# Optimization experiments

Measured on AMD Instinct MI355X. Metric: run time of the kernel, lower is better.

Reference implementation:

```python
import jax, jax.numpy as jnp
import numpy as np

N, E, F, H, O = 50000, 800000, 64, 128, 64
GRID_SIZE, SPLINE_ORDER = 3, 2


def make_grid(in_features, grid_size=GRID_SIZE, spline_order=SPLINE_ORDER, grid_range=(-1.0, 1.0)):
    h = (grid_range[1] - grid_range[0]) / grid_size
    pts = jnp.arange(-spline_order, grid_size + spline_order + 1, dtype=jnp.float32) * h + grid_range[0]
    return jnp.tile(pts[None, :], (in_features, 1))  # [in, grid_size + 2*order + 1]


def b_splines(x, grid, spline_order=SPLINE_ORDER):
    # x: [B, in], grid: [in, G+2k+1] -> bases [B, in, G+k]
    xe = x[..., None]
    bases = ((xe >= grid[:, :-1]) & (xe < grid[:, 1:])).astype(x.dtype)
    for k in range(1, spline_order + 1):
        bases = ((xe - grid[:, : -(k + 1)]) / (grid[:, k:-1] - grid[:, : -(k + 1)]) * bases[..., :-1]
                 + (grid[:, k + 1:] - xe) / (grid[:, k + 1:] - grid[:, 1:-k]) * bases[..., 1:])
    return bases


def setup_inputs() -> dict:
    key = jax.random.key(0)
    ks = jax.random.split(key, 12)
    x = jax.random.normal(ks[0], (N, F), dtype=jnp.float32)
    contexts = jax.random.normal(ks[1], (E, F), dtype=jnp.float32)
    attn = jax.random.uniform(ks[2], (E,), dtype=jnp.float32)
    seg_ids = jnp.sort(jax.random.randint(ks[3], (E,), 0, N, dtype=jnp.int32))
    s = 0.05
    Wn = jax.random.normal(ks[4], (H, F), dtype=jnp.float32) * s
    bn = jnp.zeros((H,), dtype=jnp.float32)
    Wc = jax.random.normal(ks[5], (H, F), dtype=jnp.float32) * s
    bc = jnp.zeros((H,), dtype=jnp.float32)
    Wu = jax.random.normal(ks[6], (O, H), dtype=jnp.float32) * s
    bu = jnp.zeros((O,), dtype=jnp.float32)
    n_coef = GRID_SIZE + SPLINE_ORDER
    base_w = jax.random.normal(ks[7], (O, O), dtype=jnp.float32) * s
    spline_w = jax.random.normal(ks[8], (O, O, n_coef), dtype=jnp.float32) * s
    spline_scaler = jnp.ones((O, O), dtype=jnp.float32)
    grid = make_grid(O)
    return dict(x=x, contexts=contexts, attn=attn, seg_ids=seg_ids, Wn=Wn, bn=bn,
                Wc=Wc, bc=bc, Wu=Wu, bu=bu, base_w=base_w, spline_w=spline_w,
                spline_scaler=spline_scaler, grid=grid)


def reference(x, contexts, attn, seg_ids, Wn, bn, Wc, bc, Wu, bu, base_w, spline_w, spline_scaler, grid):
    n = x.shape[0]
    # per-edge context transform, attention weighting
    ctx_t = contexts @ Wc.T + bc                      # [E, H]
    weighted = ctx_t * attn[:, None]                  # [E, H]
    seg_sum = jax.ops.segment_sum(weighted, seg_ids, num_segments=n)        # [N, H]
    deg = jax.ops.segment_sum(jnp.ones_like(attn), seg_ids, num_segments=n)  # [N]
    ctx_agg = seg_sum / jnp.maximum(deg, 1.0)[:, None]  # mean over edges per node
    x_t = x @ Wn.T + bn                               # [N, H]
    upd = (x_t + ctx_agg) @ Wu.T + bu                 # [N, O]
    # KANLinear (efficient-kan): silu base path + b-spline path
    base_out = jax.nn.silu(upd) @ base_w.T            # [N, O]
    bases = b_splines(upd, grid)                      # [N, O, G+k]
    scaled_sw = spline_w * spline_scaler[..., None]   # [O, O, G+k]
    spline_out = jnp.einsum('bik,oik->bo', bases, scaled_sw)
    kan_out = base_out + spline_out
    # nodes with no contexts keep their raw features (num_features == output_dim)
    return jnp.where(deg[:, None] > 0, kan_out, x)
```

## Files before the change

kernel.cpp:

```cpp
#include <hip/hip_runtime.h>
#include <hip/hip_bf16.h>

#define NN 50000
#define NE 800000

typedef short short8 __attribute__((ext_vector_type(8)));
typedef float f32x4 __attribute__((ext_vector_type(4)));
typedef unsigned short ushort_t;

static __device__ __forceinline__ unsigned bits(float f) { return __float_as_uint(f); }
static __device__ __forceinline__ float hi_f(float v) {
  return __uint_as_float(bits(v) & 0xFFFF0000u);
}
static __device__ __forceinline__ ushort_t hi_u(float v) { return (ushort_t)(bits(v) >> 16); }
static __device__ __forceinline__ unsigned pack_hi(float v0, float v1) {
  return (bits(v0) >> 16) | (bits(v1) & 0xFFFF0000u);
}
static __device__ __forceinline__ unsigned pack_lo(float v0, float v1) {
  float l0 = v0 - hi_f(v0), l1 = v1 - hi_f(v1);
  return (bits(l0) >> 16) | (bits(l1) & 0xFFFF0000u);
}

#define MFMA(a, b, c) __builtin_amdgcn_mfma_f32_16x16x32_bf16(a, b, c, 0, 0, 0)

__global__ __launch_bounds__(256) void kA_pack_off(
    const float* __restrict__ Wn, const float* __restrict__ Wc,
    const float* __restrict__ Wu, const float* __restrict__ base_w,
    const float* __restrict__ spline_w, const float* __restrict__ scaler,
    const int* __restrict__ seg,
    ushort_t* __restrict__ p1h, ushort_t* __restrict__ p2h,
    ushort_t* __restrict__ p3h, int* __restrict__ off) {
  int t = blockIdx.x * 256 + threadIdx.x;
  if (t < 4096) {
    int l = t & 63, lm = l & 15, lk = l >> 4;
    if (t < 2048) {
      int nt = t >> 8, ks = (t >> 6) & 3;
      int h = nt * 16 + lm;
#pragma unroll
      for (int j = 0; j < 8; ++j) {
        int f = ks * 32 + lk * 8 + j;
        float v = (f < 64) ? Wn[h * 64 + f] : Wc[h * 64 + (f - 64)];
        p1h[t * 8 + j] = hi_u(v);
      }
    }
    if (t < 1024) {
      int nt = t >> 8, ks = (t >> 6) & 3;
      int o = nt * 16 + lm;
#pragma unroll
      for (int j = 0; j < 8; ++j) {
        int hh = ks * 32 + lk * 8 + j;
        p2h[t * 8 + j] = hi_u(Wu[o * 128 + hh]);
      }
    }
    if (t < 3072) {
      int nt = t / 768, ks = (t >> 6) % 12;
      int o = nt * 16 + lm;
#pragma unroll
      for (int j = 0; j < 8; ++j) {
        int k = ks * 32 + lk * 8 + j;
        int i = k / 6, c = k % 6;
        float v = (c == 0) ? base_w[o * 64 + i]
                           : spline_w[(o * 64 + i) * 5 + (c - 1)] * scaler[o * 64 + i];
        p3h[t * 8 + j] = hi_u(v);
      }
    }
  }
  int e = t;
  if (e < NE) {
    int s1 = seg[e];
    if (e == 0) {
      for (int n = 0; n <= s1; ++n) off[n] = 0;
    } else {
      int s0 = seg[e - 1];
      for (int n = s0 + 1; n <= s1; ++n) off[n] = e;
    }
    if (e == NE - 1) {
      for (int n = s1 + 1; n <= NN; ++n) off[n] = NE;
    }
  }
}

__global__ __launch_bounds__(512, 4) void k1234(
    const float* __restrict__ x,
    const float* __restrict__ contexts, const float* __restrict__ attn,
    const int* __restrict__ off,
    const float* __restrict__ bn, const float* __restrict__ bc,
    const float* __restrict__ bu,
    const ushort_t* __restrict__ p1h, const ushort_t* __restrict__ p2h,
    const ushort_t* __restrict__ p3h,
    const float* __restrict__ gridp, float* __restrict__ out) {
  __shared__ __align__(16) unsigned char arena[49152];
  __shared__ float ap[64], degl[64];
  ushort_t* Uh = (ushort_t*)arena;
  ushort_t* Ul = (ushort_t*)(arena + 16384);
  ushort_t* Th = (ushort_t*)(arena + 32768);
  ushort_t* Vh = (ushort_t*)arena;

  int tid = threadIdx.x;
  int n0 = blockIdx.x * 64;
  int w = tid >> 6, l = tid & 63;
  int wm = w >> 2, wn = w & 3;
  int lm = l & 15, lk = l >> 4;
  const short8* P1h = (const short8*)p1h;
  const short8* P2h = (const short8*)p2h;
  const short8* P3h = (const short8*)p3h;

  {
    const float4* x4 = (const float4*)x;
    int row = tid >> 3, slot = tid & 7;
    int n = n0 + row;
    float4 a = make_float4(0.f, 0.f, 0.f, 0.f), b = a;
    if (n < NN) {
      a = x4[(size_t)n * 16 + slot * 2];
      b = x4[(size_t)n * 16 + slot * 2 + 1];
    }
    uint4 hp, lp;
    hp.x = pack_hi(a.x, a.y); hp.y = pack_hi(a.z, a.w);
    hp.z = pack_hi(b.x, b.y); hp.w = pack_hi(b.z, b.w);
    lp.x = pack_lo(a.x, a.y); lp.y = pack_lo(a.z, a.w);
    lp.z = pack_lo(b.x, b.y); lp.w = pack_lo(b.z, b.w);
    int idx = (row * 128 + slot * 8) ^ ((row & 7) << 3);
    *(uint4*)&Uh[idx] = hp;
    *(uint4*)&Ul[idx] = lp;
  }

  {
    int nb = n0 + w * 8;
    int offv = 0;
    if (l < 9) offv = off[min(nb + l, NN)];
    int sub = l >> 4, fq = l & 15;
    const float4* ctx4 = (const float4*)contexts;
#pragma unroll 1
    for (int i = 0; i < 8; ++i) {
      int s = __shfl(offv, i);
      int e_end = __shfl(offv, i + 1);
      int deg_i = e_end - s;
      float4 S = make_float4(0.f, 0.f, 0.f, 0.f);
      float A = 0.f;
      if (deg_i > 0) {
        int last = e_end - 1;
        for (int e0 = s; e0 < e_end; e0 += 16) {
          float a[4];
          float4 c[4];
#pragma unroll
          for (int u = 0; u < 4; ++u) {
            int eu = e0 + 4 * u + sub;
            a[u] = (eu < e_end) ? attn[eu] : 0.f;
            c[u] = ctx4[(size_t)min(eu, last) * 16 + fq];
          }
#pragma unroll
          for (int u = 0; u < 4; ++u) {
            S.x += a[u] * c[u].x;
            S.y += a[u] * c[u].y;
            S.z += a[u] * c[u].z;
            S.w += a[u] * c[u].w;
            A += a[u];
          }
        }
      }
#pragma unroll
      for (int m = 16; m <= 32; m <<= 1) {
        S.x += __shfl_xor(S.x, m);
        S.y += __shfl_xor(S.y, m);
        S.z += __shfl_xor(S.z, m);
        S.w += __shfl_xor(S.w, m);
        A += __shfl_xor(A, m);
      }
      float deg = (float)deg_i;
      float inv = 1.f / fmaxf(deg, 1.f);
      int row = w * 8 + i;
      if (l < 16) {
        float ox = S.x * inv, oy = S.y * inv, oz = S.z * inv, ow = S.w * inv;
        uint2 hp, lp;
        hp.x = pack_hi(ox, oy);
        hp.y = pack_hi(oz, ow);
        lp.x = pack_lo(ox, oy);
        lp.y = pack_lo(oz, ow);
        int idx = (row * 128 + 64 + l * 4) ^ ((row & 7) << 3);
        *(uint2*)&Uh[idx] = hp;
        *(uint2*)&Ul[idx] = lp;
      }
      if (l == 0) { ap[row] = A * inv; degl[row] = deg; }
    }
  }

  short8 B1[2][4], B2[4];
#pragma unroll
  for (int q = 0; q < 2; ++q)
#pragma unroll
    for (int ks = 0; ks < 4; ++ks) B1[q][ks] = P1h[((2 * wn + q) * 4 + ks) * 64 + l];
#pragma unroll
  for (int ks = 0; ks < 4; ++ks) B2[ks] = P2h[(wn * 4 + ks) * 64 + l];

  __syncthreads();

  int swzA = (lm & 7) << 3;

  f32x4 acc1[2][2];
#pragma unroll
  for (int q = 0; q < 2; ++q)
#pragma unroll
    for (int ms = 0; ms < 2; ++ms) acc1[q][ms] = (f32x4){0.f, 0.f, 0.f, 0.f};
#pragma unroll
  for (int ks = 0; ks < 4; ++ks) {
    short8 ah[2], al[2];
#pragma unroll
    for (int ms = 0; ms < 2; ++ms) {
      int ai = (((2 * wm + ms) * 16 + lm) * 128 + ks * 32 + lk * 8) ^ swzA;
      ah[ms] = *(const short8*)&Uh[ai];
      al[ms] = *(const short8*)&Ul[ai];
    }
#pragma unroll
    for (int q = 0; q < 2; ++q)
#pragma unroll
      for (int ms = 0; ms < 2; ++ms) {
        acc1[q][ms] = MFMA(ah[ms], B1[q][ks], acc1[q][ms]);
        acc1[q][ms] = MFMA(al[ms], B1[q][ks], acc1[q][ms]);
      }
  }
#pragma unroll
  for (int q = 0; q < 2; ++q) {
    int h = (2 * wn + q) * 16 + lm;
    float bnv = bn[h], bcv = bc[h];
#pragma unroll
    for (int ms = 0; ms < 2; ++ms) {
#pragma unroll
      for (int r = 0; r < 4; ++r) {
        int node = (2 * wm + ms) * 16 + lk * 4 + r;
        float t = acc1[q][ms][r] + bnv + ap[node] * bcv;
        Th[(node * 128 + h) ^ ((node & 7) << 3)] = hi_u(t);
      }
    }
  }
  __syncthreads();

  short8 B3[12];
#pragma unroll
  for (int ks = 0; ks < 12; ++ks) B3[ks] = P3h[(wn * 12 + ks) * 64 + l];
  float g[8];
#pragma unroll
  for (int j = 0; j < 8; ++j) g[j] = gridp[j];
  float r1[7], r2[6];
#pragma unroll
  for (int j = 0; j < 7; ++j) r1[j] = 1.f / (g[j + 1] - g[j]);
#pragma unroll
  for (int j = 0; j < 6; ++j) r2[j] = 1.f / (g[j + 2] - g[j]);
  float buv = bu[wn * 16 + lm];

  f32x4 acc2[2];
  acc2[0] = (f32x4){0.f, 0.f, 0.f, 0.f};
  acc2[1] = (f32x4){0.f, 0.f, 0.f, 0.f};
#pragma unroll
  for (int ks = 0; ks < 4; ++ks) {
#pragma unroll
    for (int ms = 0; ms < 2; ++ms) {
      int ai = (((2 * wm + ms) * 16 + lm) * 128 + ks * 32 + lk * 8) ^ swzA;
      short8 ah = *(const short8*)&Th[ai];
      acc2[ms] = MFMA(ah, B2[ks], acc2[ms]);
    }
  }

#pragma unroll
  for (int half = 0; half < 2; ++half) {
    if (wm == half) {
#pragma unroll
      for (int ms = 0; ms < 2; ++ms) {
#pragma unroll
        for (int r = 0; r < 4; ++r) {
          float xv = acc2[ms][r] + buv;
          float sil = xv / (1.f + __expf(-xv));
          float b0[7], b1[6], b2[5];
#pragma unroll
          for (int q = 0; q < 7; ++q) b0[q] = (xv >= g[q] && xv < g[q + 1]) ? 1.f : 0.f;
#pragma unroll
          for (int q = 0; q < 6; ++q)
            b1[q] = (xv - g[q]) * r1[q] * b0[q] + (g[q + 2] - xv) * r1[q + 1] * b0[q + 1];
#pragma unroll
          for (int q = 0; q < 5; ++q)
            b2[q] = (xv - g[q]) * r2[q] * b1[q] + (g[q + 3] - xv) * r2[q + 1] * b1[q + 1];
          int ln = ms * 16 + lk * 4 + r;
          int base = ln * 392 + (wn * 16 + lm) * 6;
          *(unsigned*)&Vh[base + 0] = pack_hi(sil, b2[0]);
          *(unsigned*)&Vh[base + 2] = pack_hi(b2[1], b2[2]);
          *(unsigned*)&Vh[base + 4] = pack_hi(b2[3], b2[4]);
        }
      }
    }
    __syncthreads();

    f32x4 accK = (f32x4){0.f, 0.f, 0.f, 0.f};
#pragma unroll
    for (int ks = 0; ks < 12; ++ks) {
      short8 ah = *(const short8*)&Vh[(wm * 16 + lm) * 392 + ks * 32 + lk * 8];
      accK = MFMA(ah, B3[ks], accK);
    }
    if (half == 0) __syncthreads();

    int o = wn * 16 + lm;
#pragma unroll
    for (int r = 0; r < 4; ++r) {
      int node = half * 32 + wm * 16 + lk * 4 + r;
      int n = n0 + node;
      if (n < NN) {
        float val = accK[r];
        if (degl[node] <= 0.f) val = x[(size_t)n * 64 + o];
        out[(size_t)n * 64 + o] = val;
      }
    }
  }
}

extern "C" void kernel_launch(void* const* d_in, const int* in_sizes, int n_in,
                              void* d_out, int out_size, void* d_ws, size_t ws_size,
                              hipStream_t stream) {
  const float* x        = (const float*)d_in[0];
  const float* contexts = (const float*)d_in[1];
  const float* attn     = (const float*)d_in[2];
  const int*   seg      = (const int*)d_in[3];
  const float* Wn       = (const float*)d_in[4];
  const float* bn       = (const float*)d_in[5];
  const float* Wc       = (const float*)d_in[6];
  const float* bc       = (const float*)d_in[7];
  const float* Wu       = (const float*)d_in[8];
  const float* bu       = (const float*)d_in[9];
  const float* base_w   = (const float*)d_in[10];
  const float* spline_w = (const float*)d_in[11];
  const float* scaler   = (const float*)d_in[12];
  const float* gridp    = (const float*)d_in[13];
  float* out = (float*)d_out;

  ushort_t* us  = (ushort_t*)d_ws;
  ushort_t* p1h = us;
  ushort_t* p2h = p1h + 16384;
  ushort_t* p3h = p2h + 8192;
  int*   off    = (int*)(p3h + 24576);

  kA_pack_off<<<3125, 256, 0, stream>>>(Wn, Wc, Wu, base_w, spline_w, scaler, seg,
                                        p1h, p2h, p3h, off);
  k1234<<<782, 512, 0, stream>>>(x, contexts, attn, off, bn, bc, bu,
                                 p1h, p2h, p3h, gridp, out);
}
```

Baseline: 67.49 us.

## Trim lo-split MFMAs, stream B operands, swizzle V tile, stage output through LDS

Lowers the launch_bounds occupancy hint from 4 to 3 blocks per CU and stops holding the B1 and B3 weight fragments in registers, loading them per k-step instead. It drops the low-part bf16 correction for the aggregated-context half of the first GEMM, keeping it only for the x half. The V tile gets a narrower XOR-swizzled row stride to cut LDS bank conflicts. The final output is staged through LDS so it can be written with coalesced float4 stores. Together these aim to lower register pressure and memory-write cost, at the price of extra global loads of weights inside the MFMA loops, some precision loss on the context path, and an extra barrier per half.

```diff
diff --git a/kernel.cpp b/kernel.cpp
--- a/kernel.cpp
+++ b/kernel.cpp
@@ -80,7 +80,7 @@
   }
 }
 
-__global__ __launch_bounds__(512, 4) void k1234(
+__global__ __launch_bounds__(512, 3) void k1234(
     const float* __restrict__ x,
     const float* __restrict__ contexts, const float* __restrict__ attn,
     const int* __restrict__ off,
@@ -95,6 +95,7 @@
   ushort_t* Ul = (ushort_t*)(arena + 16384);
   ushort_t* Th = (ushort_t*)(arena + 32768);
   ushort_t* Vh = (ushort_t*)arena;
+  float*    ot = (float*)(arena + 24576);
 
   int tid = threadIdx.x;
   int n0 = blockIdx.x * 64;
@@ -171,52 +172,45 @@
       int row = w * 8 + i;
       if (l < 16) {
         float ox = S.x * inv, oy = S.y * inv, oz = S.z * inv, ow = S.w * inv;
-        uint2 hp, lp;
+        uint2 hp;
         hp.x = pack_hi(ox, oy);
         hp.y = pack_hi(oz, ow);
-        lp.x = pack_lo(ox, oy);
-        lp.y = pack_lo(oz, ow);
         int idx = (row * 128 + 64 + l * 4) ^ ((row & 7) << 3);
         *(uint2*)&Uh[idx] = hp;
-        *(uint2*)&Ul[idx] = lp;
       }
       if (l == 0) { ap[row] = A * inv; degl[row] = deg; }
     }
   }
 
-  short8 B1[2][4], B2[4];
+  short8 B2[4];
+#pragma unroll
+  for (int ks = 0; ks < 4; ++ks) B2[ks] = P2h[(wn * 4 + ks) * 64 + l];
+
+  __syncthreads();
+
+  int swzA = (lm & 7) << 3;
+
+  f32x4 acc1[2][2];
 #pragma unroll
   for (int q = 0; q < 2; ++q)
 #pragma unroll
-    for (int ks = 0; ks < 4; ++ks) B1[q][ks] = P1h[((2 * wn + q) * 4 + ks) * 64 + l];
-#pragma unroll
-  for (int ks = 0; ks < 4; ++ks) B2[ks] = P2h[(wn * 4 + ks) * 64 + l];
-
-  __syncthreads();
-
-  int swzA = (lm & 7) << 3;
-
-  f32x4 acc1[2][2];
-#pragma unroll
-  for (int q = 0; q < 2; ++q)
-#pragma unroll
     for (int ms = 0; ms < 2; ++ms) acc1[q][ms] = (f32x4){0.f, 0.f, 0.f, 0.f};
 #pragma unroll
   for (int ks = 0; ks < 4; ++ks) {
-    short8 ah[2], al[2];
+    short8 bh0 = P1h[((2 * wn + 0) * 4 + ks) * 64 + l];
+    short8 bh1 = P1h[((2 * wn + 1) * 4 + ks) * 64 + l];
 #pragma unroll
     for (int ms = 0; ms < 2; ++ms) {
       int ai = (((2 * wm + ms) * 16 + lm) * 128 + ks * 32 + lk * 8) ^ swzA;
-      ah[ms] = *(const short8*)&Uh[ai];
-      al[ms] = *(const short8*)&Ul[ai];
-    }
-#pragma unroll
-    for (int q = 0; q < 2; ++q)
-#pragma unroll
-      for (int ms = 0; ms < 2; ++ms) {
-        acc1[q][ms] = MFMA(ah[ms], B1[q][ks], acc1[q][ms]);
-        acc1[q][ms] = MFMA(al[ms], B1[q][ks], acc1[q][ms]);
-      }
+      short8 ah = *(const short8*)&Uh[ai];
+      acc1[0][ms] = MFMA(ah, bh0, acc1[0][ms]);
+      acc1[1][ms] = MFMA(ah, bh1, acc1[1][ms]);
+      if (ks < 2) {
+        short8 al = *(const short8*)&Ul[ai];
+        acc1[0][ms] = MFMA(al, bh0, acc1[0][ms]);
+        acc1[1][ms] = MFMA(al, bh1, acc1[1][ms]);
+      }
+    }
   }
 #pragma unroll
   for (int q = 0; q < 2; ++q) {
@@ -234,9 +228,6 @@
   }
   __syncthreads();
 
-  short8 B3[12];
-#pragma unroll
-  for (int ks = 0; ks < 12; ++ks) B3[ks] = P3h[(wn * 12 + ks) * 64 + l];
   float g[8];
 #pragma unroll
   for (int j = 0; j < 8; ++j) g[j] = gridp[j];
@@ -279,10 +270,11 @@
           for (int q = 0; q < 5; ++q)
             b2[q] = (xv - g[q]) * r2[q] * b1[q] + (g[q + 3] - xv) * r2[q + 1] * b1[q + 1];
           int ln = ms * 16 + lk * 4 + r;
-          int base = ln * 392 + (wn * 16 + lm) * 6;
-          *(unsigned*)&Vh[base + 0] = pack_hi(sil, b2[0]);
-          *(unsigned*)&Vh[base + 2] = pack_hi(b2[1], b2[2]);
-          *(unsigned*)&Vh[base + 4] = pack_hi(b2[3], b2[4]);
+          int base = ln * 384 + (wn * 16 + lm) * 6;
+          int sw = (ln & 7) << 3;
+          *(unsigned*)&Vh[(base + 0) ^ sw] = pack_hi(sil, b2[0]);
+          *(unsigned*)&Vh[(base + 2) ^ sw] = pack_hi(b2[1], b2[2]);
+          *(unsigned*)&Vh[(base + 4) ^ sw] = pack_hi(b2[3], b2[4]);
         }
       }
     }
@@ -291,20 +283,32 @@
     f32x4 accK = (f32x4){0.f, 0.f, 0.f, 0.f};
 #pragma unroll
     for (int ks = 0; ks < 12; ++ks) {
-      short8 ah = *(const short8*)&Vh[(wm * 16 + lm) * 392 + ks * 32 + lk * 8];
-      accK = MFMA(ah, B3[ks], accK);
-    }
-    if (half == 0) __syncthreads();
-
-    int o = wn * 16 + lm;
-#pragma unroll
-    for (int r = 0; r < 4; ++r) {
-      int node = half * 32 + wm * 16 + lk * 4 + r;
+      short8 bh = P3h[(wn * 12 + ks) * 64 + l];
+      int ri = ((wm * 16 + lm) * 384 + ks * 32 + lk * 8) ^ swzA;
+      short8 ah = *(const short8*)&Vh[ri];
+      accK = MFMA(ah, bh, accK);
+    }
+    {
+      int o = wn * 16 + lm;
+#pragma unroll
+      for (int r = 0; r < 4; ++r) {
+        int ln = wm * 16 + lk * 4 + r;
+        ot[(ln * 64 + o) ^ ((ln & 7) << 3)] = accK[r];
+      }
+    }
+    __syncthreads();
+
+    {
+      int row2 = tid >> 4, c4 = (tid & 15) * 4;
+      int node = half * 32 + row2;
       int n = n0 + node;
       if (n < NN) {
-        float val = accK[r];
-        if (degl[node] <= 0.f) val = x[(size_t)n * 64 + o];
-        out[(size_t)n * 64 + o] = val;
+        int sw = (row2 & 7) << 3;
+        float4 v0 = *(float4*)&ot[((row2 * 64 + c4) ^ sw)];
+        if (degl[node] <= 0.f) {
+          v0 = *(const float4*)(x + (size_t)n * 64 + c4);
+        }
+        *(float4*)(out + (size_t)n * 64 + c4) = v0;
       }
     }
   }
```

Result: no change. 66.98 us (-0.8%).
